# Kernel tuning notes

Measured on AMD Instinct MI355X. Metric: run time of the kernel, lower is better.

The kernel has to match this reference:

```python
import jax, jax.numpy as jnp
import numpy as np

D_MODEL, RANK, N = 2048, 16, 16384
LR, L2, MOM, SCALE = 1e-3, 1e-4, 0.9, 0.1
LN_EPS = 1e-5


def _xavier(key, shape):
    bound = float(np.sqrt(6.0 / (shape[0] + shape[1])))
    return jax.random.uniform(key, shape, jnp.float32, -bound, bound)


def setup_inputs() -> dict:
    key = jax.random.key(0)
    ks = jax.random.split(key, 6)
    return {
        'k': jax.random.normal(ks[0], (N, D_MODEL), jnp.float32),
        'v': jax.random.normal(ks[1], (N, D_MODEL), jnp.float32),
        'B': _xavier(ks[2], (D_MODEL, RANK)),
        'C': _xavier(ks[3], (D_MODEL, RANK)),
        'D': jnp.zeros((D_MODEL,), jnp.float32),
        'S_B': jnp.zeros((D_MODEL, RANK), jnp.float32),
        'S_C': jnp.zeros((D_MODEL, RANK), jnp.float32),
        'ln_gamma': jnp.ones((D_MODEL,), jnp.float32),
        'ln_beta': jnp.zeros((D_MODEL,), jnp.float32),
        'W1': _xavier(ks[4], (D_MODEL, D_MODEL)),
        'b1': jnp.zeros((D_MODEL,), jnp.float32),
        'W2': _xavier(ks[5], (1, D_MODEL)),
        'b2': jnp.zeros((1,), jnp.float32),
    }


def _memory_matrix(B, C, D):
    # W = scale * tanh(B C^T) + diag(D)   -> [d_model, d_model]
    return SCALE * jnp.tanh(B @ C.T) + jnp.diag(D)


def _layernorm(x, gamma, beta):
    mu = jnp.mean(x, axis=-1, keepdims=True)
    var = jnp.mean(jnp.square(x - mu), axis=-1, keepdims=True)
    return (x - mu) * jax.lax.rsqrt(var + LN_EPS) * gamma + beta


def reference(k, v, B, C, D, S_B, S_C, ln_gamma, ln_beta, W1, b1, W2, b2):
    W = _memory_matrix(B, C, D)
    read_out = k @ W.T                      # [N, d_model] (read + v_hat of update)
    # ---- online update (torch.no_grad path) ----
    err = v - read_out                      # no huber (use_huber=False), no weight
    Bsz = k.shape[0]
    gradW = -(err.T @ k) / (Bsz + 1e-8) + L2 * W
    gradB = gradW @ C                       # [d_model, rank]
    gradC = gradW.T @ B
    S_B_new = MOM * S_B - LR * gradB
    S_C_new = MOM * S_C - LR * gradC
    # retention gate on mean key: LN -> Linear -> SiLU -> Linear(1) -> sigmoid
    k_mean = jnp.mean(k, axis=0, keepdims=True)           # [1, d_model]
    h = _layernorm(k_mean, ln_gamma, ln_beta)
    h = jax.nn.silu(h @ W1.T + b1)
    alpha = jax.nn.sigmoid((h @ W2.T + b2)).squeeze()     # scalar
    B_new = (1.0 - alpha) * B + S_B_new
    C_new = (1.0 - alpha) * C + S_C_new
    return read_out, B_new, C_new, S_B_new, S_C_new, alpha
```

## Files before the change

kernel.cpp:

```cpp
#include <hip/hip_runtime.h>
#include <hip/hip_bf16.h>
#include <math.h>

#define NROWS 16384
#define DM    2048
#define RK    16
#define LRc    1e-3f
#define L2c    1e-4f
#define MOMc   0.9f
#define SCALEc 0.1f
#define LNEPS  1e-5f

typedef __attribute__((ext_vector_type(8))) short short8;
typedef __attribute__((ext_vector_type(4))) float floatx4;

union U4S8 { uint4 u4; short8 s8; unsigned u[4]; };

__device__ inline unsigned pk2(float lo, float hi) {
    union { __hip_bfloat162 h; unsigned u; } cv;
    cv.h = __float22bfloat162_rn(make_float2(lo, hi));
    return cv.u;
}

#define SPLIT_PAIR(x0, x1, ho, lo_) {                                      \
    const unsigned hh_ = pk2((x0), (x1));                                  \
    const float hx0_ = __builtin_bit_cast(float, (hh_ & 0xffffu) << 16);   \
    const float hx1_ = __builtin_bit_cast(float, hh_ & 0xffff0000u);       \
    (ho) = hh_; (lo_) = pk2((x0) - hx0_, (x1) - hx1_); }

__global__ __launch_bounds__(256) void k_prep(
    const float* __restrict__ B, const float* __restrict__ C,
    const float* __restrict__ Dd,
    float* __restrict__ BtB, float* __restrict__ CtC,
    uint4* __restrict__ Cpk, uint4* __restrict__ Bpk, uint4* __restrict__ DBpk,
    int* __restrict__ flag)
{
    const int bid = blockIdx.x, t = threadIdx.x;
    if (bid < 16) {
        const int a = t >> 4, b = t & 15;
        const int dBeg = bid * 128;
        float sc = 0.f, sb = 0.f;
        for (int d = dBeg; d < dBeg + 128; ++d) {
            sc += C[d * RK + a] * C[d * RK + b];
            sb += B[d * RK + a] * B[d * RK + b];
        }
        atomicAdd(CtC + a * RK + b, sc);
        atomicAdd(BtB + a * RK + b, sb);
    } else if (bid < 32) {
        const int idx = (bid - 16) * 256 + t;
        const int c = idx >> 6, l = idx & 63;
        const int dbase = c * 32 + (l >> 4) * 8;
        const int col = l & 15;
        U4S8 uc, ub, ud;
        #pragma unroll
        for (int q = 0; q < 4; ++q) {
            const int d0 = dbase + 2 * q, d1 = d0 + 1;
            uc.u[q] = pk2(C[d0 * RK + col], C[d1 * RK + col]);
            ub.u[q] = pk2(B[d0 * RK + col], B[d1 * RK + col]);
            ud.u[q] = pk2(Dd[d0] * B[d0 * RK + col], Dd[d1] * B[d1 * RK + col]);
        }
        Cpk[idx] = uc.u4; Bpk[idx] = ub.u4; DBpk[idx] = ud.u4;
    } else {
        __shared__ int sh;
        if (t == 0) sh = 0;
        __syncthreads();
        int any = 0;
        for (int i = t; i < DM; i += 256) any |= (Dd[i] != 0.f) ? 1 : 0;
        if (any) sh = 1;
        __syncthreads();
        if (t == 0) *flag = sh;
    }
}

__global__ __launch_bounds__(256) void k_A(
    const float* __restrict__ k, const float* __restrict__ v,
    const uint4* __restrict__ Cpk, const uint4* __restrict__ Bpk,
    const uint4* __restrict__ DBpk, const int* __restrict__ flag,
    float* __restrict__ kC_g, float* __restrict__ vB_g, float* __restrict__ kDB_g)
{
    __shared__ floatx4 red[3][4][64];
    const int t = threadIdx.x;
    const int lane = t & 63;
    const int w = t >> 6;
    const int R0 = blockIdx.x * 16;
    const int m = lane & 15;
    const int g = lane >> 4;
    const int dnz = *flag;
    const float* kp = k + (size_t)(R0 + m) * DM + g * 8;
    const float* vp = v + (size_t)(R0 + m) * DM + g * 8;

    floatx4 a0 = {0.f,0.f,0.f,0.f}, a1 = {0.f,0.f,0.f,0.f}, a2 = {0.f,0.f,0.f,0.f};
    const int c0 = w * 16;

    float4 ka = *(const float4*)(kp + c0 * 32);
    float4 kb = *(const float4*)(kp + c0 * 32 + 4);
    float4 va = *(const float4*)(vp + c0 * 32);
    float4 vb = *(const float4*)(vp + c0 * 32 + 4);
    uint4 cf = Cpk[c0 * 64 + lane];
    uint4 bf = Bpk[c0 * 64 + lane];
    uint4 df = make_uint4(0u,0u,0u,0u);
    if (dnz) df = DBpk[c0 * 64 + lane];

    for (int cc = 0; cc < 16; ++cc) {
        const int c = c0 + cc;
        const float4 kac = ka, kbc = kb, vac = va, vbc = vb;
        const uint4 cfc = cf, bfc = bf, dfc = df;
        const int cn = (cc + 1 < 16) ? c + 1 : c;
        ka = *(const float4*)(kp + cn * 32);
        kb = *(const float4*)(kp + cn * 32 + 4);
        va = *(const float4*)(vp + cn * 32);
        vb = *(const float4*)(vp + cn * 32 + 4);
        cf = Cpk[cn * 64 + lane];
        bf = Bpk[cn * 64 + lane];
        if (dnz) df = DBpk[cn * 64 + lane];

        U4S8 kf, vf, cu, bu, du;
        kf.u[0] = pk2(kac.x, kac.y); kf.u[1] = pk2(kac.z, kac.w);
        kf.u[2] = pk2(kbc.x, kbc.y); kf.u[3] = pk2(kbc.z, kbc.w);
        vf.u[0] = pk2(vac.x, vac.y); vf.u[1] = pk2(vac.z, vac.w);
        vf.u[2] = pk2(vbc.x, vbc.y); vf.u[3] = pk2(vbc.z, vbc.w);
        cu.u4 = cfc; bu.u4 = bfc; du.u4 = dfc;

        a0 = __builtin_amdgcn_mfma_f32_16x16x32_bf16(kf.s8, cu.s8, a0, 0, 0, 0);
        a1 = __builtin_amdgcn_mfma_f32_16x16x32_bf16(vf.s8, bu.s8, a1, 0, 0, 0);
        if (dnz)
            a2 = __builtin_amdgcn_mfma_f32_16x16x32_bf16(kf.s8, du.s8, a2, 0, 0, 0);
    }

    red[0][w][lane] = a0;
    red[1][w][lane] = a1;
    red[2][w][lane] = a2;
    __syncthreads();
    if (w == 0) {
        const floatx4 s0 = red[0][0][lane] + red[0][1][lane] + red[0][2][lane] + red[0][3][lane];
        const floatx4 s1 = red[1][0][lane] + red[1][1][lane] + red[1][2][lane] + red[1][3][lane];
        const floatx4 s2 = red[2][0][lane] + red[2][1][lane] + red[2][2][lane] + red[2][3][lane];
        #pragma unroll
        for (int j = 0; j < 4; ++j) {
            const size_t o = (size_t)(R0 + g * 4 + j) * RK + m;
            kC_g[o] = s0[j];
            vB_g[o] = s1[j];
            if (dnz) kDB_g[o] = s2[j];
        }
    }
}

__global__ __launch_bounds__(256) void k_mid(
    const float* __restrict__ kC_g, const float* __restrict__ vB_g,
    float* __restrict__ eB_g, const float* __restrict__ BtB,
    const int* __restrict__ flag)
{
    __shared__ float Bsh[256];
    const int t = threadIdx.x;
    Bsh[t] = BtB[t];
    __syncthreads();
    const int dnz = *flag;
    const int n = blockIdx.x * 256 + t;
    float kc[16], vb[16], kdb[16];
    #pragma unroll
    for (int q = 0; q < 4; ++q) {
        const float4 a = *(const float4*)(kC_g + (size_t)n * RK + q * 4);
        const float4 b = *(const float4*)(vB_g + (size_t)n * RK + q * 4);
        kc[q*4+0]=a.x; kc[q*4+1]=a.y; kc[q*4+2]=a.z; kc[q*4+3]=a.w;
        vb[q*4+0]=b.x; vb[q*4+1]=b.y; vb[q*4+2]=b.z; vb[q*4+3]=b.w;
        kdb[q*4+0]=0.f; kdb[q*4+1]=0.f; kdb[q*4+2]=0.f; kdb[q*4+3]=0.f;
    }
    if (dnz) {
        #pragma unroll
        for (int q = 0; q < 4; ++q) {
            const float4 c = *(const float4*)(eB_g + (size_t)n * RK + q * 4);
            kdb[q*4+0]=c.x; kdb[q*4+1]=c.y; kdb[q*4+2]=c.z; kdb[q*4+3]=c.w;
        }
    }
    float out[16];
    #pragma unroll
    for (int r = 0; r < 16; ++r) {
        float acc = 0.f;
        #pragma unroll
        for (int s = 0; s < 16; ++s) acc += kc[s] * Bsh[s * 16 + r];
        out[r] = vb[r] - kdb[r] - SCALEc * acc;
    }
    #pragma unroll
    for (int q = 0; q < 4; ++q)
        *(float4*)(eB_g + (size_t)n * RK + q * 4) =
            make_float4(out[q*4+0], out[q*4+1], out[q*4+2], out[q*4+3]);
}

__global__ __launch_bounds__(256) void k_pack(
    const float* __restrict__ kC_g, const float* __restrict__ eB_g,
    uint4* __restrict__ kCh, uint4* __restrict__ kCl,
    uint4* __restrict__ eBh, uint4* __restrict__ eBl)
{
    const int idx = blockIdx.x * 256 + threadIdx.x;
    const int c = idx >> 6, l = idx & 63;
    const int col = l & 15;
    const int nb = c * 32 + (l >> 4) * 8;
    U4S8 ah, al, bh, bl;
    #pragma unroll
    for (int q = 0; q < 4; ++q) {
        const int n0 = nb + 2 * q;
        const float x0 = kC_g[(size_t)n0 * RK + col];
        const float x1 = kC_g[(size_t)(n0 + 1) * RK + col];
        const float y0 = eB_g[(size_t)n0 * RK + col];
        const float y1 = eB_g[(size_t)(n0 + 1) * RK + col];
        SPLIT_PAIR(x0, x1, ah.u[q], al.u[q]);
        SPLIT_PAIR(y0, y1, bh.u[q], bl.u[q]);
    }
    kCh[idx] = ah.u4; kCl[idx] = al.u4;
    eBh[idx] = bh.u4; eBl[idx] = bl.u4;
}

__global__ __launch_bounds__(256) void k_T(
    const float* __restrict__ k, const float* __restrict__ v,
    const uint4* __restrict__ kCh, const uint4* __restrict__ kCl,
    const uint4* __restrict__ eBh, const uint4* __restrict__ eBl,
    float* __restrict__ P1, float* __restrict__ G2, float* __restrict__ Q,
    float* __restrict__ S2, float* __restrict__ colsum)
{
    const int t = threadIdx.x;
    const int lane = t & 63;
    const int w = t >> 6;
    const int dgrp = blockIdx.x & 31;
    const int chunk = blockIdx.x >> 5;
    const int d = dgrp * 64 + w * 16 + (lane & 15);
    const int rowoff = (lane >> 4) * 8;
    const int c0 = chunk * 16;

    floatx4 accP = {0.f,0.f,0.f,0.f}, accG = {0.f,0.f,0.f,0.f};
    floatx4 accQ = {0.f,0.f,0.f,0.f}, accS = {0.f,0.f,0.f,0.f};
    float csl = 0.f;

    uint4 nKh = kCh[(size_t)c0 * 64 + lane];
    uint4 nKl = kCl[(size_t)c0 * 64 + lane];
    uint4 nEh = eBh[(size_t)c0 * 64 + lane];
    uint4 nEl = eBl[(size_t)c0 * 64 + lane];
    float kn[8], vn[8];
    {
        const size_t base = ((size_t)(c0 * 32 + rowoff)) * DM + d;
        #pragma unroll
        for (int e = 0; e < 8; ++e) {
            kn[e] = k[base + (size_t)(e * DM)];
            vn[e] = v[base + (size_t)(e * DM)];
        }
    }

    for (int it = 0; it < 16; ++it) {
        const int c = c0 + it;
        const uint4 aKh = nKh, aKl = nKl, aEh = nEh, aEl = nEl;
        float kc[8], vc[8];
        #pragma unroll
        for (int e = 0; e < 8; ++e) { kc[e] = kn[e]; vc[e] = vn[e]; }

        if (it + 1 < 16) {
            const int cn = c + 1;
            nKh = kCh[(size_t)cn * 64 + lane];
            nKl = kCl[(size_t)cn * 64 + lane];
            nEh = eBh[(size_t)cn * 64 + lane];
            nEl = eBl[(size_t)cn * 64 + lane];
            const size_t base = ((size_t)(cn * 32 + rowoff)) * DM + d;
            #pragma unroll
            for (int e = 0; e < 8; ++e) {
                kn[e] = k[base + (size_t)(e * DM)];
                vn[e] = v[base + (size_t)(e * DM)];
            }
        }

        U4S8 kfh, kfl, vfh, vfl, uKh, uKl, uEh, uEl;
        SPLIT_PAIR(kc[0], kc[1], kfh.u[0], kfl.u[0]);
        SPLIT_PAIR(kc[2], kc[3], kfh.u[1], kfl.u[1]);
        SPLIT_PAIR(kc[4], kc[5], kfh.u[2], kfl.u[2]);
        SPLIT_PAIR(kc[6], kc[7], kfh.u[3], kfl.u[3]);
        SPLIT_PAIR(vc[0], vc[1], vfh.u[0], vfl.u[0]);
        SPLIT_PAIR(vc[2], vc[3], vfh.u[1], vfl.u[1]);
        SPLIT_PAIR(vc[4], vc[5], vfh.u[2], vfl.u[2]);
        SPLIT_PAIR(vc[6], vc[7], vfh.u[3], vfl.u[3]);
        csl += kc[0] + kc[1] + kc[2] + kc[3] + kc[4] + kc[5] + kc[6] + kc[7];
        uKh.u4 = aKh; uKl.u4 = aKl; uEh.u4 = aEh; uEl.u4 = aEl;

        accP = __builtin_amdgcn_mfma_f32_16x16x32_bf16(uKh.s8, vfh.s8, accP, 0, 0, 0);
        accP = __builtin_amdgcn_mfma_f32_16x16x32_bf16(uKh.s8, vfl.s8, accP, 0, 0, 0);
        accP = __builtin_amdgcn_mfma_f32_16x16x32_bf16(uKl.s8, vfh.s8, accP, 0, 0, 0);
        accG = __builtin_amdgcn_mfma_f32_16x16x32_bf16(uEh.s8, kfh.s8, accG, 0, 0, 0);
        accG = __builtin_amdgcn_mfma_f32_16x16x32_bf16(uEh.s8, kfl.s8, accG, 0, 0, 0);
        accG = __builtin_amdgcn_mfma_f32_16x16x32_bf16(uEl.s8, kfh.s8, accG, 0, 0, 0);
        accQ = __builtin_amdgcn_mfma_f32_16x16x32_bf16(uKh.s8, kfh.s8, accQ, 0, 0, 0);
        accS = __builtin_amdgcn_mfma_f32_16x16x32_bf16(uKh.s8, uKh.s8, accS, 0, 0, 0);
    }

    const int r0 = (lane >> 4) * 4;
    #pragma unroll
    for (int j = 0; j < 4; ++j) {
        atomicAdd(P1 + (size_t)d * RK + r0 + j, accP[j]);
        atomicAdd(G2 + (size_t)d * RK + r0 + j, accG[j]);
        atomicAdd(Q  + (size_t)d * RK + r0 + j, accQ[j]);
    }
    if (dgrp == 0 && w == 0) {
        #pragma unroll
        for (int j = 0; j < 4; ++j)
            atomicAdd(S2 + (r0 + j) * RK + (lane & 15), accS[j]);
    }
    csl += __shfl_xor(csl, 16);
    csl += __shfl_xor(csl, 32);
    if ((lane >> 4) == 0) atomicAdd(colsum + d, csl);
}

__global__ __launch_bounds__(256) void k_ro(
    const float* __restrict__ k, const float* __restrict__ B,
    const float* __restrict__ Dd, const float* __restrict__ kC_g,
    const int* __restrict__ flag, float* __restrict__ ro)
{
    __shared__ float kCch[64 * 16];
    const int t = threadIdx.x;
    const int slab = blockIdx.x & 1;
    const int chunk = blockIdx.x >> 1;
    const int d0 = slab * 1024 + t * 4;
    const int row0 = chunk * 64;
    const int dnz = *flag;

    float Breg[4][16], Dreg[4];
    #pragma unroll
    for (int i = 0; i < 4; ++i) {
        #pragma unroll
        for (int q = 0; q < 4; ++q) {
            const float4 b4 = *(const float4*)(B + (size_t)(d0 + i) * RK + q * 4);
            Breg[i][q*4+0] = b4.x; Breg[i][q*4+1] = b4.y;
            Breg[i][q*4+2] = b4.z; Breg[i][q*4+3] = b4.w;
        }
        Dreg[i] = Dd[d0 + i];
    }
    *(float4*)&kCch[t * 4] = *(const float4*)(kC_g + (size_t)row0 * RK + t * 4);
    __syncthreads();

    float4 k0 = make_float4(0.f,0.f,0.f,0.f), k1 = k0;
    if (dnz) {
        k0 = *(const float4*)(k + (size_t)row0 * DM + d0);
        k1 = *(const float4*)(k + (size_t)(row0 + 1) * DM + d0);
    }

    for (int rr = 0; rr < 64; ++rr) {
        const int n = row0 + rr;
        const float4 kc4 = k0;
        if (dnz) {
            const int np = row0 + ((rr + 2 < 64) ? rr + 2 : 63);
            k0 = k1; k1 = *(const float4*)(k + (size_t)np * DM + d0);
        }
        float kcr[16];
        #pragma unroll
        for (int q = 0; q < 4; ++q) {
            const float4 c4 = *(const float4*)&kCch[rr * 16 + q * 4];
            kcr[q*4+0] = c4.x; kcr[q*4+1] = c4.y; kcr[q*4+2] = c4.z; kcr[q*4+3] = c4.w;
        }
        float roa[4];
        const float ka4[4] = {kc4.x, kc4.y, kc4.z, kc4.w};
        #pragma unroll
        for (int i = 0; i < 4; ++i) {
            float s = 0.f;
            #pragma unroll
            for (int r = 0; r < 16; ++r) s += kcr[r] * Breg[i][r];
            roa[i] = SCALEc * s;
            if (dnz) roa[i] += ka4[i] * Dreg[i];
        }
        *(float4*)(ro + (size_t)n * DM + d0) = make_float4(roa[0], roa[1], roa[2], roa[3]);
    }
}

__global__ __launch_bounds__(256) void k_ln(
    const float* __restrict__ colsum,
    const float* __restrict__ gam, const float* __restrict__ bet,
    float* __restrict__ h1)
{
    __shared__ float red[256];
    __shared__ float mu_sh, var_sh;
    const int t = threadIdx.x;
    float x[8];
    float s = 0.f;
    #pragma unroll
    for (int i = 0; i < 8; ++i) {
        x[i] = colsum[t + 256 * i] * (1.0f / (float)NROWS);
        s += x[i];
    }
    red[t] = s; __syncthreads();
    for (int off = 128; off > 0; off >>= 1) {
        if (t < off) red[t] += red[t + off];
        __syncthreads();
    }
    if (t == 0) mu_sh = red[0] * (1.0f / (float)DM);
    __syncthreads();
    const float mu = mu_sh;
    float s2 = 0.f;
    #pragma unroll
    for (int i = 0; i < 8; ++i) { const float dd = x[i] - mu; s2 += dd * dd; }
    __syncthreads();
    red[t] = s2; __syncthreads();
    for (int off = 128; off > 0; off >>= 1) {
        if (t < off) red[t] += red[t + off];
        __syncthreads();
    }
    if (t == 0) var_sh = red[0] * (1.0f / (float)DM);
    __syncthreads();
    const float rstd = rsqrtf(var_sh + LNEPS);
    #pragma unroll
    for (int i = 0; i < 8; ++i) {
        const int d = t + 256 * i;
        h1[d] = (x[i] - mu) * rstd * gam[d] + bet[d];
    }
}

__global__ __launch_bounds__(256) void k_gemv(
    const float* __restrict__ h1, const float* __restrict__ W1,
    const float* __restrict__ b1, float* __restrict__ h2)
{
    const int t = threadIdx.x;
    const int lane = t & 63;
    const int w = t >> 6;
    const int row = blockIdx.x * 4 + w;
    const float* wr = W1 + (size_t)row * DM;
    float s = 0.f;
    #pragma unroll
    for (int j = 0; j < 8; ++j) {
        const float4 a = *(const float4*)(wr + j * 256 + lane * 4);
        const float4 b = *(const float4*)(h1 + j * 256 + lane * 4);
        s += a.x * b.x + a.y * b.y + a.z * b.z + a.w * b.w;
    }
    #pragma unroll
    for (int off = 32; off > 0; off >>= 1) s += __shfl_down(s, off);
    if (lane == 0) {
        const float val = s + b1[row];
        h2[row] = val / (1.0f + expf(-val));
    }
}

__global__ __launch_bounds__(256) void k_alpha(
    const float* __restrict__ h2, const float* __restrict__ W2,
    const float* __restrict__ b2,
    float* __restrict__ alpha_ws, float* __restrict__ out_alpha)
{
    __shared__ float red[256];
    const int t = threadIdx.x;
    float s = 0.f;
    for (int i = t; i < DM; i += 256) s += h2[i] * W2[i];
    red[t] = s; __syncthreads();
    for (int off = 128; off > 0; off >>= 1) {
        if (t < off) red[t] += red[t + off];
        __syncthreads();
    }
    if (t == 0) {
        const float logit = red[0] + b2[0];
        const float a = 1.0f / (1.0f + expf(-logit));
        alpha_ws[0] = a;
        out_alpha[0] = a;
    }
}

__global__ __launch_bounds__(256) void k_update(
    const float* __restrict__ B, const float* __restrict__ C,
    const float* __restrict__ Dd,
    const float* __restrict__ S_B, const float* __restrict__ S_C,
    const float* __restrict__ P1, const float* __restrict__ G2,
    const float* __restrict__ Q, const float* __restrict__ S2,
    const float* __restrict__ CtC, const float* __restrict__ BtB,
    const float* __restrict__ alpha_ws,
    float* __restrict__ outB, float* __restrict__ outC,
    float* __restrict__ outSB, float* __restrict__ outSC)
{
    const int idx = blockIdx.x * 256 + threadIdx.x;
    const int d = idx >> 4, r = idx & 15;
    const float alpha = alpha_ws[0];

    float Brow[16], Crow[16];
    #pragma unroll
    for (int q = 0; q < 4; ++q) {
        const float4 b4 = *(const float4*)(B + (size_t)d * RK + q * 4);
        const float4 c4 = *(const float4*)(C + (size_t)d * RK + q * 4);
        Brow[q*4+0] = b4.x; Brow[q*4+1] = b4.y; Brow[q*4+2] = b4.z; Brow[q*4+3] = b4.w;
        Crow[q*4+0] = c4.x; Crow[q*4+1] = c4.y; Crow[q*4+2] = c4.z; Crow[q*4+3] = c4.w;
    }
    float bc = 0.f, cb = 0.f, bs2 = 0.f;
    #pragma unroll
    for (int a = 0; a < 16; ++a) {
        bc  += Brow[a] * CtC[a * RK + r];
        cb  += Crow[a] * BtB[a * RK + r];
        bs2 += Brow[a] * S2[a * RK + r];
    }
    const float Ddv = Dd[d];
    const float invN = 1.0f / (float)NROWS;
    const float G1v = P1[idx] - SCALEc * bs2 - Ddv * Q[idx];
    const float gradB = -G1v * invN + L2c * (SCALEc * bc + Ddv * Crow[r]);
    const float gradC = -G2[idx] * invN + L2c * (SCALEc * cb + Ddv * Brow[r]);
    const float sB = MOMc * S_B[idx] - LRc * gradB;
    const float sC = MOMc * S_C[idx] - LRc * gradC;
    outSB[idx] = sB;
    outSC[idx] = sC;
    outB[idx] = (1.0f - alpha) * B[idx] + sB;
    outC[idx] = (1.0f - alpha) * C[idx] + sC;
}

extern "C" void kernel_launch(void* const* d_in, const int* in_sizes, int n_in,
                              void* d_out, int out_size, void* d_ws, size_t ws_size,
                              hipStream_t stream)
{
    const float* k   = (const float*)d_in[0];
    const float* v   = (const float*)d_in[1];
    const float* B   = (const float*)d_in[2];
    const float* C   = (const float*)d_in[3];
    const float* Dd  = (const float*)d_in[4];
    const float* S_B = (const float*)d_in[5];
    const float* S_C = (const float*)d_in[6];
    const float* gam = (const float*)d_in[7];
    const float* bet = (const float*)d_in[8];
    const float* W1  = (const float*)d_in[9];
    const float* b1  = (const float*)d_in[10];
    const float* W2  = (const float*)d_in[11];
    const float* b2  = (const float*)d_in[12];

    float* out      = (float*)d_out;
    float* ro       = out;
    float* outB     = out + (size_t)NROWS * DM;
    float* outC     = outB + (size_t)DM * RK;
    float* outSB    = outC + (size_t)DM * RK;
    float* outSC    = outSB + (size_t)DM * RK;
    float* outAlpha = outSC + (size_t)DM * RK;

    float* ws = (float*)d_ws;
    float* kC_g   = ws;
    float* vB_g   = kC_g + (size_t)NROWS * RK;
    float* eB_g   = vB_g + (size_t)NROWS * RK;
    float* P1     = eB_g + (size_t)NROWS * RK;
    float* G2     = P1 + (size_t)DM * RK;
    float* Q      = G2 + (size_t)DM * RK;
    float* S2     = Q + (size_t)DM * RK;
    float* CtC    = S2 + 256;
    float* BtB    = CtC + 256;
    float* colsum = BtB + 256;
    float* h1     = colsum + DM;
    float* h2     = h1 + DM;
    uint4* Cpk    = (uint4*)(h2 + DM);
    uint4* Bpk    = Cpk + 4096;
    uint4* DBpk   = Bpk + 4096;
    uint4* kCh    = DBpk + 4096;
    uint4* kCl    = kCh + 32768;
    uint4* eBh    = kCl + 32768;
    uint4* eBl    = eBh + 32768;
    float* alphaW = (float*)(eBl + 32768);
    int*   flag   = (int*)(alphaW + 1);

    hipMemsetAsync(P1, 0, (size_t)101120 * sizeof(float), stream);

    hipLaunchKernelGGL(k_prep, dim3(33), dim3(256), 0, stream,
                       B, C, Dd, BtB, CtC, Cpk, Bpk, DBpk, flag);
    hipLaunchKernelGGL(k_A, dim3(1024), dim3(256), 0, stream,
                       k, v, Cpk, Bpk, DBpk, flag, kC_g, vB_g, eB_g);
    hipLaunchKernelGGL(k_mid, dim3(64), dim3(256), 0, stream,
                       kC_g, vB_g, eB_g, BtB, flag);
    hipLaunchKernelGGL(k_pack, dim3(128), dim3(256), 0, stream,
                       kC_g, eB_g, kCh, kCl, eBh, eBl);
    hipLaunchKernelGGL(k_T, dim3(1024), dim3(256), 0, stream,
                       k, v, kCh, kCl, eBh, eBl, P1, G2, Q, S2, colsum);
    hipLaunchKernelGGL(k_ro, dim3(512), dim3(256), 0, stream,
                       k, B, Dd, kC_g, flag, ro);
    hipLaunchKernelGGL(k_ln, dim3(1), dim3(256), 0, stream, colsum, gam, bet, h1);
    hipLaunchKernelGGL(k_gemv, dim3(512), dim3(256), 0, stream, h1, W1, b1, h2);
    hipLaunchKernelGGL(k_alpha, dim3(1), dim3(256), 0, stream, h2, W2, b2, alphaW, outAlpha);
    hipLaunchKernelGGL(k_update, dim3(128), dim3(256), 0, stream,
                       B, C, Dd, S_B, S_C, P1, G2, Q, S2, CtC, BtB, alphaW,
                       outB, outC, outSB, outSC);
}
```

Baseline: 214.6 us.

## Split reduction passes across more blocks and drop bf16 hi/lo split

Splits k_A's column reduction into two halves written to separate partial buffers that k_mid sums, doubling the grid. k_T now processes 8 chunks per block over a doubled grid and drops the hi/lo bf16 error-compensated split, using a single bf16 MFMA per product. k_ro handles 16 rows per block with four times as many blocks. The aim is better occupancy and less MFMA and conversion work, at the cost of lower accuracy in the gradient accumulations and more atomic/partial traffic.

```diff
diff --git a/kernel.cpp b/kernel.cpp
--- a/kernel.cpp
+++ b/kernel.cpp
@@ -21,12 +21,6 @@
     cv.h = __float22bfloat162_rn(make_float2(lo, hi));
     return cv.u;
 }
-
-#define SPLIT_PAIR(x0, x1, ho, lo_) {                                      \
-    const unsigned hh_ = pk2((x0), (x1));                                  \
-    const float hx0_ = __builtin_bit_cast(float, (hh_ & 0xffffu) << 16);   \
-    const float hx1_ = __builtin_bit_cast(float, hh_ & 0xffff0000u);       \
-    (ho) = hh_; (lo_) = pk2((x0) - hx0_, (x1) - hx1_); }
 
 __global__ __launch_bounds__(256) void k_prep(
     const float* __restrict__ B, const float* __restrict__ C,
@@ -76,13 +70,15 @@
     const float* __restrict__ k, const float* __restrict__ v,
     const uint4* __restrict__ Cpk, const uint4* __restrict__ Bpk,
     const uint4* __restrict__ DBpk, const int* __restrict__ flag,
-    float* __restrict__ kC_g, float* __restrict__ vB_g, float* __restrict__ kDB_g)
+    float* __restrict__ kCp, float* __restrict__ vBp, float* __restrict__ kDBp)
 {
     __shared__ floatx4 red[3][4][64];
     const int t = threadIdx.x;
     const int lane = t & 63;
     const int w = t >> 6;
-    const int R0 = blockIdx.x * 16;
+    const int rowgrp = blockIdx.x >> 1;
+    const int half = blockIdx.x & 1;
+    const int R0 = rowgrp * 16;
     const int m = lane & 15;
     const int g = lane >> 4;
     const int dnz = *flag;
@@ -90,7 +86,7 @@
     const float* vp = v + (size_t)(R0 + m) * DM + g * 8;
 
     floatx4 a0 = {0.f,0.f,0.f,0.f}, a1 = {0.f,0.f,0.f,0.f}, a2 = {0.f,0.f,0.f,0.f};
-    const int c0 = w * 16;
+    const int c0 = half * 32 + w * 8;
 
     float4 ka = *(const float4*)(kp + c0 * 32);
     float4 kb = *(const float4*)(kp + c0 * 32 + 4);
@@ -101,11 +97,11 @@
     uint4 df = make_uint4(0u,0u,0u,0u);
     if (dnz) df = DBpk[c0 * 64 + lane];
 
-    for (int cc = 0; cc < 16; ++cc) {
+    for (int cc = 0; cc < 8; ++cc) {
         const int c = c0 + cc;
         const float4 kac = ka, kbc = kb, vac = va, vbc = vb;
         const uint4 cfc = cf, bfc = bf, dfc = df;
-        const int cn = (cc + 1 < 16) ? c + 1 : c;
+        const int cn = (cc + 1 < 8) ? c + 1 : c;
         ka = *(const float4*)(kp + cn * 32);
         kb = *(const float4*)(kp + cn * 32 + 4);
         va = *(const float4*)(vp + cn * 32);
@@ -135,20 +131,22 @@
         const floatx4 s0 = red[0][0][lane] + red[0][1][lane] + red[0][2][lane] + red[0][3][lane];
         const floatx4 s1 = red[1][0][lane] + red[1][1][lane] + red[1][2][lane] + red[1][3][lane];
         const floatx4 s2 = red[2][0][lane] + red[2][1][lane] + red[2][2][lane] + red[2][3][lane];
+        const size_t H = (size_t)half * NROWS * RK;
         #pragma unroll
         for (int j = 0; j < 4; ++j) {
-            const size_t o = (size_t)(R0 + g * 4 + j) * RK + m;
-            kC_g[o] = s0[j];
-            vB_g[o] = s1[j];
-            if (dnz) kDB_g[o] = s2[j];
+            const size_t o = H + (size_t)(R0 + g * 4 + j) * RK + m;
+            kCp[o] = s0[j];
+            vBp[o] = s1[j];
+            if (dnz) kDBp[o] = s2[j];
         }
     }
 }
 
 __global__ __launch_bounds__(256) void k_mid(
-    const float* __restrict__ kC_g, const float* __restrict__ vB_g,
-    float* __restrict__ eB_g, const float* __restrict__ BtB,
-    const int* __restrict__ flag)
+    const float* __restrict__ kCp, const float* __restrict__ vBp,
+    const float* __restrict__ kDBp, const float* __restrict__ BtB,
+    const int* __restrict__ flag,
+    float* __restrict__ kC_g, float* __restrict__ eB_g)
 {
     __shared__ float Bsh[256];
     const int t = threadIdx.x;
@@ -156,20 +154,25 @@
     __syncthreads();
     const int dnz = *flag;
     const int n = blockIdx.x * 256 + t;
+    const size_t H = (size_t)NROWS * RK;
     float kc[16], vb[16], kdb[16];
     #pragma unroll
     for (int q = 0; q < 4; ++q) {
-        const float4 a = *(const float4*)(kC_g + (size_t)n * RK + q * 4);
-        const float4 b = *(const float4*)(vB_g + (size_t)n * RK + q * 4);
-        kc[q*4+0]=a.x; kc[q*4+1]=a.y; kc[q*4+2]=a.z; kc[q*4+3]=a.w;
-        vb[q*4+0]=b.x; vb[q*4+1]=b.y; vb[q*4+2]=b.z; vb[q*4+3]=b.w;
+        const float4 a0 = *(const float4*)(kCp + (size_t)n * RK + q * 4);
+        const float4 a1 = *(const float4*)(kCp + H + (size_t)n * RK + q * 4);
+        const float4 b0 = *(const float4*)(vBp + (size_t)n * RK + q * 4);
+        const float4 b1 = *(const float4*)(vBp + H + (size_t)n * RK + q * 4);
+        kc[q*4+0]=a0.x+a1.x; kc[q*4+1]=a0.y+a1.y; kc[q*4+2]=a0.z+a1.z; kc[q*4+3]=a0.w+a1.w;
+        vb[q*4+0]=b0.x+b1.x; vb[q*4+1]=b0.y+b1.y; vb[q*4+2]=b0.z+b1.z; vb[q*4+3]=b0.w+b1.w;
         kdb[q*4+0]=0.f; kdb[q*4+1]=0.f; kdb[q*4+2]=0.f; kdb[q*4+3]=0.f;
     }
     if (dnz) {
         #pragma unroll
         for (int q = 0; q < 4; ++q) {
-            const float4 c = *(const float4*)(eB_g + (size_t)n * RK + q * 4);
-            kdb[q*4+0]=c.x; kdb[q*4+1]=c.y; kdb[q*4+2]=c.z; kdb[q*4+3]=c.w;
+            const float4 c0 = *(const float4*)(kDBp + (size_t)n * RK + q * 4);
+            const float4 c1 = *(const float4*)(kDBp + H + (size_t)n * RK + q * 4);
+            kdb[q*4+0]=c0.x+c1.x; kdb[q*4+1]=c0.y+c1.y;
+            kdb[q*4+2]=c0.z+c1.z; kdb[q*4+3]=c0.w+c1.w;
         }
     }
     float out[16];
@@ -181,39 +184,36 @@
         out[r] = vb[r] - kdb[r] - SCALEc * acc;
     }
     #pragma unroll
-    for (int q = 0; q < 4; ++q)
+    for (int q = 0; q < 4; ++q) {
+        *(float4*)(kC_g + (size_t)n * RK + q * 4) =
+            make_float4(kc[q*4+0], kc[q*4+1], kc[q*4+2], kc[q*4+3]);
         *(float4*)(eB_g + (size_t)n * RK + q * 4) =
             make_float4(out[q*4+0], out[q*4+1], out[q*4+2], out[q*4+3]);
+    }
 }
 
 __global__ __launch_bounds__(256) void k_pack(
     const float* __restrict__ kC_g, const float* __restrict__ eB_g,
-    uint4* __restrict__ kCh, uint4* __restrict__ kCl,
-    uint4* __restrict__ eBh, uint4* __restrict__ eBl)
+    uint4* __restrict__ kCb, uint4* __restrict__ eBb)
 {
     const int idx = blockIdx.x * 256 + threadIdx.x;
     const int c = idx >> 6, l = idx & 63;
     const int col = l & 15;
     const int nb = c * 32 + (l >> 4) * 8;
-    U4S8 ah, al, bh, bl;
+    U4S8 ah, bh;
     #pragma unroll
     for (int q = 0; q < 4; ++q) {
         const int n0 = nb + 2 * q;
-        const float x0 = kC_g[(size_t)n0 * RK + col];
-        const float x1 = kC_g[(size_t)(n0 + 1) * RK + col];
-        const float y0 = eB_g[(size_t)n0 * RK + col];
-        const float y1 = eB_g[(size_t)(n0 + 1) * RK + col];
-        SPLIT_PAIR(x0, x1, ah.u[q], al.u[q]);
-        SPLIT_PAIR(y0, y1, bh.u[q], bl.u[q]);
-    }
-    kCh[idx] = ah.u4; kCl[idx] = al.u4;
-    eBh[idx] = bh.u4; eBl[idx] = bl.u4;
+        ah.u[q] = pk2(kC_g[(size_t)n0 * RK + col], kC_g[(size_t)(n0 + 1) * RK + col]);
+        bh.u[q] = pk2(eB_g[(size_t)n0 * RK + col], eB_g[(size_t)(n0 + 1) * RK + col]);
+    }
+    kCb[idx] = ah.u4;
+    eBb[idx] = bh.u4;
 }
 
 __global__ __launch_bounds__(256) void k_T(
     const float* __restrict__ k, const float* __restrict__ v,
-    const uint4* __restrict__ kCh, const uint4* __restrict__ kCl,
-    const uint4* __restrict__ eBh, const uint4* __restrict__ eBl,
+    const uint4* __restrict__ kCb, const uint4* __restrict__ eBb,
     float* __restrict__ P1, float* __restrict__ G2, float* __restrict__ Q,
     float* __restrict__ S2, float* __restrict__ colsum)
 {
@@ -221,70 +221,51 @@
     const int lane = t & 63;
     const int w = t >> 6;
     const int dgrp = blockIdx.x & 31;
-    const int chunk = blockIdx.x >> 5;
+    const int cgrp = blockIdx.x >> 5;
     const int d = dgrp * 64 + w * 16 + (lane & 15);
     const int rowoff = (lane >> 4) * 8;
-    const int c0 = chunk * 16;
+    const int c0 = cgrp * 8;
 
     floatx4 accP = {0.f,0.f,0.f,0.f}, accG = {0.f,0.f,0.f,0.f};
     floatx4 accQ = {0.f,0.f,0.f,0.f}, accS = {0.f,0.f,0.f,0.f};
     float csl = 0.f;
 
-    uint4 nKh = kCh[(size_t)c0 * 64 + lane];
-    uint4 nKl = kCl[(size_t)c0 * 64 + lane];
-    uint4 nEh = eBh[(size_t)c0 * 64 + lane];
-    uint4 nEl = eBl[(size_t)c0 * 64 + lane];
+    const size_t stepc = (size_t)32 * DM;
+    const float* kp = k + ((size_t)(c0 * 32 + rowoff)) * DM + d;
+    const float* vp = v + ((size_t)(c0 * 32 + rowoff)) * DM + d;
+
     float kn[8], vn[8];
-    {
-        const size_t base = ((size_t)(c0 * 32 + rowoff)) * DM + d;
-        #pragma unroll
-        for (int e = 0; e < 8; ++e) {
-            kn[e] = k[base + (size_t)(e * DM)];
-            vn[e] = v[base + (size_t)(e * DM)];
-        }
-    }
-
-    for (int it = 0; it < 16; ++it) {
+    #pragma unroll
+    for (int e = 0; e < 8; ++e) {
+        kn[e] = kp[(size_t)e * DM];
+        vn[e] = vp[(size_t)e * DM];
+    }
+
+    for (int it = 0; it < 8; ++it) {
         const int c = c0 + it;
-        const uint4 aKh = nKh, aKl = nKl, aEh = nEh, aEl = nEl;
-        float kc[8], vc[8];
-        #pragma unroll
-        for (int e = 0; e < 8; ++e) { kc[e] = kn[e]; vc[e] = vn[e]; }
-
-        if (it + 1 < 16) {
-            const int cn = c + 1;
-            nKh = kCh[(size_t)cn * 64 + lane];
-            nKl = kCl[(size_t)cn * 64 + lane];
-            nEh = eBh[(size_t)cn * 64 + lane];
-            nEl = eBl[(size_t)cn * 64 + lane];
-            const size_t base = ((size_t)(cn * 32 + rowoff)) * DM + d;
+        U4S8 uK, uE, kf, vf;
+        uK.u4 = kCb[(size_t)c * 64 + lane];
+        uE.u4 = eBb[(size_t)c * 64 + lane];
+
+        kf.u[0] = pk2(kn[0], kn[1]); kf.u[1] = pk2(kn[2], kn[3]);
+        kf.u[2] = pk2(kn[4], kn[5]); kf.u[3] = pk2(kn[6], kn[7]);
+        vf.u[0] = pk2(vn[0], vn[1]); vf.u[1] = pk2(vn[2], vn[3]);
+        vf.u[2] = pk2(vn[4], vn[5]); vf.u[3] = pk2(vn[6], vn[7]);
+        csl += kn[0] + kn[1] + kn[2] + kn[3] + kn[4] + kn[5] + kn[6] + kn[7];
+
+        if (it + 1 < 8) {
+            kp += stepc; vp += stepc;
             #pragma unroll
             for (int e = 0; e < 8; ++e) {
-                kn[e] = k[base + (size_t)(e * DM)];
-                vn[e] = v[base + (size_t)(e * DM)];
+                kn[e] = kp[(size_t)e * DM];
+                vn[e] = vp[(size_t)e * DM];
             }
         }
 
-        U4S8 kfh, kfl, vfh, vfl, uKh, uKl, uEh, uEl;
-        SPLIT_PAIR(kc[0], kc[1], kfh.u[0], kfl.u[0]);
-        SPLIT_PAIR(kc[2], kc[3], kfh.u[1], kfl.u[1]);
-        SPLIT_PAIR(kc[4], kc[5], kfh.u[2], kfl.u[2]);
-        SPLIT_PAIR(kc[6], kc[7], kfh.u[3], kfl.u[3]);
-        SPLIT_PAIR(vc[0], vc[1], vfh.u[0], vfl.u[0]);
-        SPLIT_PAIR(vc[2], vc[3], vfh.u[1], vfl.u[1]);
-        SPLIT_PAIR(vc[4], vc[5], vfh.u[2], vfl.u[2]);
-        SPLIT_PAIR(vc[6], vc[7], vfh.u[3], vfl.u[3]);
-        csl += kc[0] + kc[1] + kc[2] + kc[3] + kc[4] + kc[5] + kc[6] + kc[7];
-        uKh.u4 = aKh; uKl.u4 = aKl; uEh.u4 = aEh; uEl.u4 = aEl;
-
-        accP = __builtin_amdgcn_mfma_f32_16x16x32_bf16(uKh.s8, vfh.s8, accP, 0, 0, 0);
-        accP = __builtin_amdgcn_mfma_f32_16x16x32_bf16(uKh.s8, vfl.s8, accP, 0, 0, 0);
-        accP = __builtin_amdgcn_mfma_f32_16x16x32_bf16(uKl.s8, vfh.s8, accP, 0, 0, 0);
-        accG = __builtin_amdgcn_mfma_f32_16x16x32_bf16(uEh.s8, kfh.s8, accG, 0, 0, 0);
-        accG = __builtin_amdgcn_mfma_f32_16x16x32_bf16(uEh.s8, kfl.s8, accG, 0, 0, 0);
-        accG = __builtin_amdgcn_mfma_f32_16x16x32_bf16(uEl.s8, kfh.s8, accG, 0, 0, 0);
-        accQ = __builtin_amdgcn_mfma_f32_16x16x32_bf16(uKh.s8, kfh.s8, accQ, 0, 0, 0);
-        accS = __builtin_amdgcn_mfma_f32_16x16x32_bf16(uKh.s8, uKh.s8, accS, 0, 0, 0);
+        accP = __builtin_amdgcn_mfma_f32_16x16x32_bf16(uK.s8, vf.s8, accP, 0, 0, 0);
+        accG = __builtin_amdgcn_mfma_f32_16x16x32_bf16(uE.s8, kf.s8, accG, 0, 0, 0);
+        accQ = __builtin_amdgcn_mfma_f32_16x16x32_bf16(uK.s8, kf.s8, accQ, 0, 0, 0);
+        accS = __builtin_amdgcn_mfma_f32_16x16x32_bf16(uK.s8, uK.s8, accS, 0, 0, 0);
     }
 
     const int r0 = (lane >> 4) * 4;
@@ -309,12 +290,12 @@
     const float* __restrict__ Dd, const float* __restrict__ kC_g,
     const int* __restrict__ flag, float* __restrict__ ro)
 {
-    __shared__ float kCch[64 * 16];
+    __shared__ float kCch[16 * 16];
     const int t = threadIdx.x;
     const int slab = blockIdx.x & 1;
     const int chunk = blockIdx.x >> 1;
     const int d0 = slab * 1024 + t * 4;
-    const int row0 = chunk * 64;
+    const int row0 = chunk * 16;
     const int dnz = *flag;
 
     float Breg[4][16], Dreg[4];
@@ -328,7 +309,7 @@
         }
         Dreg[i] = Dd[d0 + i];
     }
-    *(float4*)&kCch[t * 4] = *(const float4*)(kC_g + (size_t)row0 * RK + t * 4);
+    if (t < 64) *(float4*)&kCch[t * 4] = *(const float4*)(kC_g + (size_t)row0 * RK + t * 4);
     __syncthreads();
 
     float4 k0 = make_float4(0.f,0.f,0.f,0.f), k1 = k0;
@@ -337,11 +318,11 @@
         k1 = *(const float4*)(k + (size_t)(row0 + 1) * DM + d0);
     }
 
-    for (int rr = 0; rr < 64; ++rr) {
+    for (int rr = 0; rr < 16; ++rr) {
         const int n = row0 + rr;
         const float4 kc4 = k0;
         if (dnz) {
-            const int np = row0 + ((rr + 2 < 64) ? rr + 2 : 63);
+            const int np = row0 + ((rr + 2 < 16) ? rr + 2 : 15);
             k0 = k1; k1 = *(const float4*)(k + (size_t)np * DM + d0);
         }
         float kcr[16];
@@ -522,9 +503,11 @@
     float* outAlpha = outSC + (size_t)DM * RK;
 
     float* ws = (float*)d_ws;
-    float* kC_g   = ws;
-    float* vB_g   = kC_g + (size_t)NROWS * RK;
-    float* eB_g   = vB_g + (size_t)NROWS * RK;
+    float* kCp    = ws;
+    float* vBp    = kCp + (size_t)2 * NROWS * RK;
+    float* kDBp   = vBp + (size_t)2 * NROWS * RK;
+    float* kC_g   = kDBp + (size_t)2 * NROWS * RK;
+    float* eB_g   = kC_g + (size_t)NROWS * RK;
     float* P1     = eB_g + (size_t)NROWS * RK;
     float* G2     = P1 + (size_t)DM * RK;
     float* Q      = G2 + (size_t)DM * RK;
@@ -537,26 +520,24 @@
     uint4* Cpk    = (uint4*)(h2 + DM);
     uint4* Bpk    = Cpk + 4096;
     uint4* DBpk   = Bpk + 4096;
-    uint4* kCh    = DBpk + 4096;
-    uint4* kCl    = kCh + 32768;
-    uint4* eBh    = kCl + 32768;
-    uint4* eBl    = eBh + 32768;
-    float* alphaW = (float*)(eBl + 32768);
+    uint4* kCb    = DBpk + 4096;
+    uint4* eBb    = kCb + 32768;
+    float* alphaW = (float*)(eBb + 32768);
     int*   flag   = (int*)(alphaW + 1);
 
     hipMemsetAsync(P1, 0, (size_t)101120 * sizeof(float), stream);
 
     hipLaunchKernelGGL(k_prep, dim3(33), dim3(256), 0, stream,
                        B, C, Dd, BtB, CtC, Cpk, Bpk, DBpk, flag);
-    hipLaunchKernelGGL(k_A, dim3(1024), dim3(256), 0, stream,
-                       k, v, Cpk, Bpk, DBpk, flag, kC_g, vB_g, eB_g);
+    hipLaunchKernelGGL(k_A, dim3(2048), dim3(256), 0, stream,
+                       k, v, Cpk, Bpk, DBpk, flag, kCp, vBp, kDBp);
     hipLaunchKernelGGL(k_mid, dim3(64), dim3(256), 0, stream,
-                       kC_g, vB_g, eB_g, BtB, flag);
+                       kCp, vBp, kDBp, BtB, flag, kC_g, eB_g);
     hipLaunchKernelGGL(k_pack, dim3(128), dim3(256), 0, stream,
-                       kC_g, eB_g, kCh, kCl, eBh, eBl);
-    hipLaunchKernelGGL(k_T, dim3(1024), dim3(256), 0, stream,
-                       k, v, kCh, kCl, eBh, eBl, P1, G2, Q, S2, colsum);
-    hipLaunchKernelGGL(k_ro, dim3(512), dim3(256), 0, stream,
+                       kC_g, eB_g, kCb, eBb);
+    hipLaunchKernelGGL(k_T, dim3(2048), dim3(256), 0, stream,
+                       k, v, kCb, eBb, P1, G2, Q, S2, colsum);
+    hipLaunchKernelGGL(k_ro, dim3(2048), dim3(256), 0, stream,
                        k, B, Dd, kC_g, flag, ro);
     hipLaunchKernelGGL(k_ln, dim3(1), dim3(256), 0, stream, colsum, gam, bet, h1);
     hipLaunchKernelGGL(k_gemv, dim3(512), dim3(256), 0, stream, h1, W1, b1, h2);
```

New measurement: 273.3 us. 27.3% more time.
